# Kernel tuning notes

Measured on AMD Instinct MI355X. Metric: run time of the kernel, lower is better.

The kernel has to match this reference:

```python
import jax, jax.numpy as jnp
import numpy as np

BATCH, DIN, DSTATE, DOUT = 16384, 1024, 2048, 1024


def setup_inputs() -> dict:
    key = jax.random.key(0)
    ks = jax.random.split(key, 8)
    return {
        "u_in": jax.random.normal(ks[0], (BATCH, 1, DIN), dtype=jnp.float32),
        "x_re": jnp.zeros((DSTATE,), dtype=jnp.float32),
        "x_im": jnp.zeros((DSTATE,), dtype=jnp.float32),
        "nu_log": jax.random.uniform(ks[1], (DSTATE,), dtype=jnp.float32),
        "theta_log": jax.random.uniform(ks[2], (DSTATE,), dtype=jnp.float32),
        "gamma_log": jax.random.uniform(ks[3], (DSTATE,), dtype=jnp.float32),
        "B_re": jax.random.normal(ks[4], (DSTATE, DIN), dtype=jnp.float32) / np.sqrt(2 * DIN).astype(np.float32),
        "B_im": jax.random.normal(ks[5], (DSTATE, DIN), dtype=jnp.float32) / np.sqrt(2 * DIN).astype(np.float32),
        "C_re": jax.random.normal(ks[6], (DOUT, DSTATE), dtype=jnp.float32) / np.sqrt(DSTATE).astype(np.float32),
        "C_im": jax.random.normal(ks[7], (DOUT, DSTATE), dtype=jnp.float32) / np.sqrt(DSTATE).astype(np.float32),
        "D": jax.random.normal(jax.random.fold_in(key, 99), (DOUT, DIN), dtype=jnp.float32) / np.sqrt(DIN).astype(np.float32),
    }


def reference(u_in, x_re, x_im, nu_log, theta_log, gamma_log, B_re, B_im, C_re, C_im, D):
    # Diagonal complex transition lambda = exp(-exp(nu_log)) * exp(i*exp(theta_log))
    lam_mod = jnp.exp(-jnp.exp(nu_log))            # [S]
    theta = jnp.exp(theta_log)                     # [S]
    lam_re = lam_mod * jnp.cos(theta)
    lam_im = lam_mod * jnp.sin(theta)
    gammas = jnp.exp(gamma_log)                    # [S]
    # Bu = B @ u (u is real, so complex matmul splits into two real GEMMs)
    Bu_re = jnp.einsum('boi,si->bos', u_in, B_re)  # [B,1,S]
    Bu_im = jnp.einsum('boi,si->bos', u_in, B_im)  # [B,1,S]
    # x_new = lambda * x + gamma * Bu   (complex, diagonal)
    xn_re = lam_re * x_re - lam_im * x_im + gammas * Bu_re
    xn_im = lam_re * x_im + lam_im * x_re + gammas * Bu_im
    # y = 2*Re(C @ x_new) + D @ u
    y = (2.0 * (jnp.einsum('bos,js->boj', xn_re, C_re)
                - jnp.einsum('bos,js->boj', xn_im, C_im))
         + jnp.einsum('boi,ji->boj', u_in, D))     # [B,1,O]
    return y
```

## Files before the change

### kernel.cpp

```cpp
#include <hip/hip_runtime.h>
#include <hip/hip_fp16.h>
#include <stdint.h>


typedef _Float16 f16x8 __attribute__((ext_vector_type(8)));
typedef float f32x4 __attribute__((ext_vector_type(4)));

#define GLOBAL_AS __attribute__((address_space(1)))
#define LDS_AS __attribute__((address_space(3)))

constexpr int BATCH = 16384, DIN = 1024, DSTATE = 2048, DOUT = 1024;
constexpr int S2 = 2 * DSTATE;

__device__ __forceinline__ int lds_off(int row, int k) {
  int slot = k >> 3;
  int sl = slot ^ ((row >> 1) & 3);
  return row * 64 + sl * 16 + (k & 7) * 2;
}

__global__ void k_bgt(const float* __restrict__ Bre, const float* __restrict__ Bim,
                      const float* __restrict__ ga, __half* __restrict__ Bh,
                      __half* __restrict__ Bl) {
  __shared__ float tile[32][33];
  int s0 = blockIdx.x * 32, i0 = blockIdx.y * 32;
  int c = threadIdx.x & 31, r0 = threadIdx.x >> 5;
  const float* src = (s0 < DSTATE) ? Bre : Bim;
  int sbase = (s0 < DSTATE) ? s0 : s0 - DSTATE;
  for (int rr = 0; rr < 32; rr += 8) {
    int s = sbase + r0 + rr;
    tile[r0 + rr][c] = src[(long)s * DIN + i0 + c] * (256.f * expf(ga[s]));
  }
  __syncthreads();
  for (int rr = 0; rr < 32; rr += 8) {
    int i = i0 + r0 + rr;
    float v = tile[c][r0 + rr];
    __half h = __float2half(v);
    __half l = __float2half(v - __half2float(h));
    Bh[(long)i * S2 + s0 + c] = h;
    Bl[(long)i * S2 + s0 + c] = l;
  }
}

__global__ void k_y0(const float* __restrict__ xr, const float* __restrict__ xi,
                     const float* __restrict__ nu, const float* __restrict__ th,
                     const float* __restrict__ Cre, const float* __restrict__ Cim,
                     float* __restrict__ y0) {
  int j = blockIdx.x;
  float acc = 0.f;
  for (int s = threadIdx.x; s < DSTATE; s += 256) {
    float lm = expf(-expf(nu[s]));
    float t = expf(th[s]);
    float lr = lm * cosf(t), li = lm * sinf(t);
    float cr = lr * xr[s] - li * xi[s];
    float ci = lr * xi[s] + li * xr[s];
    acc += cr * Cre[(long)j * DSTATE + s] - ci * Cim[(long)j * DSTATE + s];
  }
  for (int off = 32; off; off >>= 1) acc += __shfl_down(acc, off);
  __shared__ float red[4];
  if ((threadIdx.x & 63) == 0) red[threadIdx.x >> 6] = acc;
  __syncthreads();
  if (threadIdx.x == 0) y0[j] = 2.f * (red[0] + red[1] + red[2] + red[3]);
}

template <int BM, int BN, int AMODE, int EPI>
__global__ __launch_bounds__(256, 4) void k_gemm(
    const float* __restrict__ A, const float* __restrict__ A2,
    const __half* __restrict__ Bh, const __half* __restrict__ Bl,
    const float* __restrict__ extra, float* __restrict__ outF,
    int M, int N, int K, int kiters, int kchunk) {
  constexpr int FM = BM / 32;
  constexpr int FN = BN / 32;
  constexpr int ABYTES = BM * 64;
  constexpr int BBYTES = BN * 64;
  __shared__ alignas(16) char smem[ABYTES + 2 * BBYTES];
  char* sA = smem;
  char* sBh = smem + ABYTES;
  char* sBl = smem + ABYTES + BBYTES;

  const int tid = threadIdx.x;
  const int lane = tid & 63;
  const int wid = tid >> 6;
  const int wr = wid >> 1, wc = wid & 1;
  int bm0, bn0, kb;
  if constexpr (EPI == 1) {
    int wg = blockIdx.x;
    int lin = (wg & 7) * 128 + (wg >> 3);
    bm0 = (lin >> 3) * BM;
    bn0 = (lin & 7) * BN;
    kb = 0;
  } else {
    bm0 = blockIdx.y * BM;
    bn0 = blockIdx.x * BN;
    kb = blockIdx.z * kchunk;
  }
  const int r16 = lane & 15;
  const int ksl = lane >> 4;

  f32x4 acc[FM][FN];
#pragma unroll
  for (int i = 0; i < FM; ++i)
#pragma unroll
    for (int j = 0; j < FN; ++j) acc[i][j] = f32x4{0.f, 0.f, 0.f, 0.f};

  constexpr int APT = (BM * 8) / 256;
  constexpr int IPW = (BN / 16) / 4;

  for (int kt = 0; kt < kiters; ++kt) {
    __syncthreads();
#pragma unroll
    for (int it = 0; it < APT; ++it) {
      int idx = it * 256 + tid;
      int row = idx >> 3;
      int k0 = (idx & 7) * 4;
      f32x4 v;
      if constexpr (AMODE == 2) {
        v = *(const f32x4*)(A + (long)(bm0 + row) * K + kb + kt * 32 + k0);
      } else {
        int s = kb + kt * 32 + k0;
        const float* src = (s < DSTATE) ? A : A2;
        int sc = (s < DSTATE) ? s : s - DSTATE;
        v = *(const f32x4*)(src + (long)(bm0 + row) * DSTATE + sc);
        v *= (s < DSTATE) ? 512.f : -512.f;
      }
      union { __half h[4]; uint64_t u; } p;
#pragma unroll
      for (int j = 0; j < 4; ++j) p.h[j] = __float2half(v[j]);
      *(uint64_t*)(sA + lds_off(row, k0)) = p.u;
    }
#pragma unroll
    for (int ii = 0; ii < IPW; ++ii) {
      int inst = wid * IPW + ii;
      int row = inst * 16 + (lane >> 2);
      int slot = (lane & 3) ^ ((row >> 1) & 3);
      const __half* gh = Bh + (long)(bn0 + row) * K + kb + kt * 32 + slot * 8;
      const __half* gl = Bl + (long)(bn0 + row) * K + kb + kt * 32 + slot * 8;
      __builtin_amdgcn_global_load_lds((GLOBAL_AS const unsigned int*)gh,
                                       (LDS_AS unsigned int*)(sBh + inst * 1024), 16, 0, 0);
      __builtin_amdgcn_global_load_lds((GLOBAL_AS const unsigned int*)gl,
                                       (LDS_AS unsigned int*)(sBl + inst * 1024), 16, 0, 0);
    }
    __syncthreads();
    f16x8 a[FM], bh[FN], bl[FN];
#pragma unroll
    for (int m = 0; m < FM; ++m) {
      int row = wr * (BM / 2) + m * 16 + r16;
      a[m] = *(const f16x8*)(sA + lds_off(row, ksl * 8));
    }
#pragma unroll
    for (int n = 0; n < FN; ++n) {
      int row = wc * (BN / 2) + n * 16 + r16;
      bh[n] = *(const f16x8*)(sBh + lds_off(row, ksl * 8));
      bl[n] = *(const f16x8*)(sBl + lds_off(row, ksl * 8));
    }
#pragma unroll
    for (int m = 0; m < FM; ++m)
#pragma unroll
      for (int n = 0; n < FN; ++n)
        acc[m][n] = __builtin_amdgcn_mfma_f32_16x16x32_f16(a[m], bh[n], acc[m][n], 0, 0, 0);
#pragma unroll
    for (int m = 0; m < FM; ++m)
#pragma unroll
      for (int n = 0; n < FN; ++n)
        acc[m][n] = __builtin_amdgcn_mfma_f32_16x16x32_f16(a[m], bl[n], acc[m][n], 0, 0, 0);
  }

  const int rowb = (lane >> 4) * 4;
#pragma unroll
  for (int m = 0; m < FM; ++m)
#pragma unroll
    for (int n = 0; n < FN; ++n)
#pragma unroll
      for (int r = 0; r < 4; ++r) {
        int gr = bm0 + wr * (BM / 2) + m * 16 + rowb + r;
        int gc = bn0 + wc * (BN / 2) + n * 16 + r16;
        if constexpr (EPI == 0) {
          outF[(long)blockIdx.z * M * N + (long)gr * N + gc] = acc[m][n][r];
        } else {
          outF[(long)gr * N + gc] = acc[m][n][r] * (1.f / 256.f) + extra[gc];
        }
      }
}

__global__ void k_redM(const float* __restrict__ P, const float* __restrict__ D,
                       __half* __restrict__ Mh, __half* __restrict__ Ml, int nparts) {
  int idx = (blockIdx.x * 256 + threadIdx.x) * 4;
  f32x4 s = {0.f, 0.f, 0.f, 0.f};
  for (int p = 0; p < nparts; ++p)
    s += *(const f32x4*)(P + ((long)p << 20) + idx);
  f32x4 d = *(const f32x4*)(D + idx);
  union { __half h[4]; uint64_t u; } ph, pl;
#pragma unroll
  for (int j = 0; j < 4; ++j) {
    float v = s[j] * (1.f / 256.f) + 256.f * d[j];
    __half hh = __float2half(v);
    ph.h[j] = hh;
    pl.h[j] = __float2half(v - __half2float(hh));
  }
  *(uint64_t*)(Mh + idx) = ph.u;
  *(uint64_t*)(Ml + idx) = pl.u;
}

extern "C" void kernel_launch(void* const* d_in, const int* in_sizes, int n_in,
                              void* d_out, int out_size, void* d_ws, size_t ws_size,
                              hipStream_t stream) {
  const float* u   = (const float*)d_in[0];
  const float* xr  = (const float*)d_in[1];
  const float* xi  = (const float*)d_in[2];
  const float* nu  = (const float*)d_in[3];
  const float* th  = (const float*)d_in[4];
  const float* ga  = (const float*)d_in[5];
  const float* Bre = (const float*)d_in[6];
  const float* Bim = (const float*)d_in[7];
  const float* Cre = (const float*)d_in[8];
  const float* Cim = (const float*)d_in[9];
  const float* Dm  = (const float*)d_in[10];
  float* y = (float*)d_out;

  char* w = (char*)d_ws;
  float* y0  = (float*)(w);
  __half* Bgh = (__half*)(w + 65536);
  __half* Bgl = (__half*)(w + 65536 + 8388608);
  __half* Mh  = (__half*)(w + 65536 + 16777216);
  __half* Ml  = (__half*)(w + 65536 + 16777216 + 2097152);
  const size_t pbase = 65536 + 16777216 + 4194304;
  float* Mpart = (float*)(w + pbase);

  const size_t part = (size_t)DOUT * DIN * 4;
  int KS = (ws_size >= pbase + 8 * part) ? 8 : (ws_size >= pbase + 4 * part) ? 4 : 2;

  k_bgt<<<dim3(S2 / 32, DIN / 32), 256, 0, stream>>>(Bre, Bim, ga, Bgh, Bgl);
  k_y0<<<DOUT, 256, 0, stream>>>(xr, xi, nu, th, Cre, Cim, y0);
  k_gemm<128, 128, 1, 0><<<dim3(DIN / 128, DOUT / 128, KS), 256, 0, stream>>>(
      Cre, Cim, Bgh, Bgl, nullptr, Mpart, DOUT, DIN, S2, (S2 / KS) / 32, S2 / KS);
  k_redM<<<1024, 256, 0, stream>>>(Mpart, Dm, Mh, Ml, KS);
  k_gemm<128, 128, 2, 1><<<(BATCH / 128) * (DOUT / 128), 256, 0, stream>>>(
      u, nullptr, Mh, Ml, y0, y, BATCH, DOUT, DIN, DIN / 32, 0);
}
```

Before: 296.7 us.

## Double-buffer LDS tiles in GEMM with register-prefetched A and async B loads

Replaces the single-buffered GEMM kernel with a double-buffered version. While MFMAs run on the current stage, the next k-tile's A is prefetched into registers and B is issued with async global_load_lds. The A values are converted and written to the alternate buffer after compute, which cuts to one barrier per iteration. The cost is doubled LDS (48KB) and more registers, so launch bounds drop to 2 blocks per CU and occupancy may fall.

```diff
diff --git a/kernel.cpp b/kernel.cpp
--- a/kernel.cpp
+++ b/kernel.cpp
@@ -62,20 +62,59 @@
   if (threadIdx.x == 0) y0[j] = 2.f * (red[0] + red[1] + red[2] + red[3]);
 }
 
-template <int BM, int BN, int AMODE, int EPI>
-__global__ __launch_bounds__(256, 4) void k_gemm(
+template <int AMODE>
+__device__ __forceinline__ f32x4 load_a(const float* __restrict__ A,
+                                        const float* __restrict__ A2,
+                                        int bm0, int K, int kglob, int tid, int it) {
+  int idx = it * 256 + tid;
+  int row = idx >> 3;
+  int k0 = (idx & 7) * 4;
+  if constexpr (AMODE == 2) {
+    return *(const f32x4*)(A + (long)(bm0 + row) * K + kglob + k0);
+  } else {
+    int s = kglob + k0;
+    const float* src = (s < DSTATE) ? A : A2;
+    int sc = (s < DSTATE) ? s : s - DSTATE;
+    f32x4 v = *(const f32x4*)(src + (long)(bm0 + row) * DSTATE + sc);
+    return v * ((s < DSTATE) ? 512.f : -512.f);
+  }
+}
+
+__device__ __forceinline__ void write_a(f32x4 v, char* sA, int tid, int it) {
+  int idx = it * 256 + tid;
+  int row = idx >> 3;
+  int k0 = (idx & 7) * 4;
+  union { __half h[4]; uint64_t u; } p;
+#pragma unroll
+  for (int j = 0; j < 4; ++j) p.h[j] = __float2half(v[j]);
+  *(uint64_t*)(sA + lds_off(row, k0)) = p.u;
+}
+
+__device__ __forceinline__ void stage_b(const __half* __restrict__ Bh,
+                                        const __half* __restrict__ Bl,
+                                        char* sBh, char* sBl,
+                                        int bn0, int K, int kglob, int wid, int lane) {
+#pragma unroll
+  for (int ii = 0; ii < 2; ++ii) {
+    int inst = wid * 2 + ii;
+    int row = inst * 16 + (lane >> 2);
+    int slot = (lane & 3) ^ ((row >> 1) & 3);
+    const __half* gh = Bh + (long)(bn0 + row) * K + kglob + slot * 8;
+    const __half* gl = Bl + (long)(bn0 + row) * K + kglob + slot * 8;
+    __builtin_amdgcn_global_load_lds((GLOBAL_AS const unsigned int*)gh,
+                                     (LDS_AS unsigned int*)(sBh + inst * 1024), 16, 0, 0);
+    __builtin_amdgcn_global_load_lds((GLOBAL_AS const unsigned int*)gl,
+                                     (LDS_AS unsigned int*)(sBl + inst * 1024), 16, 0, 0);
+  }
+}
+
+template <int AMODE, int EPI>
+__global__ __launch_bounds__(256, 2) void k_gemm2(
     const float* __restrict__ A, const float* __restrict__ A2,
     const __half* __restrict__ Bh, const __half* __restrict__ Bl,
     const float* __restrict__ extra, float* __restrict__ outF,
-    int M, int N, int K, int kiters, int kchunk) {
-  constexpr int FM = BM / 32;
-  constexpr int FN = BN / 32;
-  constexpr int ABYTES = BM * 64;
-  constexpr int BBYTES = BN * 64;
-  __shared__ alignas(16) char smem[ABYTES + 2 * BBYTES];
-  char* sA = smem;
-  char* sBh = smem + ABYTES;
-  char* sBl = smem + ABYTES + BBYTES;
+    int K, int N, int kiters, int kchunk) {
+  __shared__ alignas(16) char smem[2 * 24576];
 
   const int tid = threadIdx.x;
   const int lane = tid & 63;
@@ -85,96 +124,78 @@
   if constexpr (EPI == 1) {
     int wg = blockIdx.x;
     int lin = (wg & 7) * 128 + (wg >> 3);
-    bm0 = (lin >> 3) * BM;
-    bn0 = (lin & 7) * BN;
+    bm0 = (lin >> 3) * 128;
+    bn0 = (lin & 7) * 128;
     kb = 0;
   } else {
-    bm0 = blockIdx.y * BM;
-    bn0 = blockIdx.x * BN;
+    bm0 = blockIdx.y * 128;
+    bn0 = blockIdx.x * 128;
     kb = blockIdx.z * kchunk;
   }
   const int r16 = lane & 15;
   const int ksl = lane >> 4;
 
-  f32x4 acc[FM][FN];
-#pragma unroll
-  for (int i = 0; i < FM; ++i)
-#pragma unroll
-    for (int j = 0; j < FN; ++j) acc[i][j] = f32x4{0.f, 0.f, 0.f, 0.f};
-
-  constexpr int APT = (BM * 8) / 256;
-  constexpr int IPW = (BN / 16) / 4;
+  f32x4 acc[4][4];
+#pragma unroll
+  for (int i = 0; i < 4; ++i)
+#pragma unroll
+    for (int j = 0; j < 4; ++j) acc[i][j] = f32x4{0.f, 0.f, 0.f, 0.f};
+
+  f32x4 va[4];
+#pragma unroll
+  for (int it = 0; it < 4; ++it) va[it] = load_a<AMODE>(A, A2, bm0, K, kb, tid, it);
+  stage_b(Bh, Bl, smem + 8192, smem + 16384, bn0, K, kb, wid, lane);
+#pragma unroll
+  for (int it = 0; it < 4; ++it) write_a(va[it], smem, tid, it);
+  __syncthreads();
 
   for (int kt = 0; kt < kiters; ++kt) {
-    __syncthreads();
-#pragma unroll
-    for (int it = 0; it < APT; ++it) {
-      int idx = it * 256 + tid;
-      int row = idx >> 3;
-      int k0 = (idx & 7) * 4;
-      f32x4 v;
-      if constexpr (AMODE == 2) {
-        v = *(const f32x4*)(A + (long)(bm0 + row) * K + kb + kt * 32 + k0);
-      } else {
-        int s = kb + kt * 32 + k0;
-        const float* src = (s < DSTATE) ? A : A2;
-        int sc = (s < DSTATE) ? s : s - DSTATE;
-        v = *(const f32x4*)(src + (long)(bm0 + row) * DSTATE + sc);
-        v *= (s < DSTATE) ? 512.f : -512.f;
-      }
-      union { __half h[4]; uint64_t u; } p;
-#pragma unroll
-      for (int j = 0; j < 4; ++j) p.h[j] = __float2half(v[j]);
-      *(uint64_t*)(sA + lds_off(row, k0)) = p.u;
+    char* cur = smem + (kt & 1) * 24576;
+    char* nxt = smem + ((kt + 1) & 1) * 24576;
+    const bool more = (kt + 1 < kiters);
+    if (more) {
+      int kg = kb + (kt + 1) * 32;
+#pragma unroll
+      for (int it = 0; it < 4; ++it) va[it] = load_a<AMODE>(A, A2, bm0, K, kg, tid, it);
+      stage_b(Bh, Bl, nxt + 8192, nxt + 16384, bn0, K, kg, wid, lane);
     }
-#pragma unroll
-    for (int ii = 0; ii < IPW; ++ii) {
-      int inst = wid * IPW + ii;
-      int row = inst * 16 + (lane >> 2);
-      int slot = (lane & 3) ^ ((row >> 1) & 3);
-      const __half* gh = Bh + (long)(bn0 + row) * K + kb + kt * 32 + slot * 8;
-      const __half* gl = Bl + (long)(bn0 + row) * K + kb + kt * 32 + slot * 8;
-      __builtin_amdgcn_global_load_lds((GLOBAL_AS const unsigned int*)gh,
-                                       (LDS_AS unsigned int*)(sBh + inst * 1024), 16, 0, 0);
-      __builtin_amdgcn_global_load_lds((GLOBAL_AS const unsigned int*)gl,
-                                       (LDS_AS unsigned int*)(sBl + inst * 1024), 16, 0, 0);
+    f16x8 a[4], bh[4], bl[4];
+#pragma unroll
+    for (int m = 0; m < 4; ++m)
+      a[m] = *(const f16x8*)(cur + lds_off(wr * 64 + m * 16 + r16, ksl * 8));
+#pragma unroll
+    for (int n = 0; n < 4; ++n) {
+      bh[n] = *(const f16x8*)(cur + 8192 + lds_off(wc * 64 + n * 16 + r16, ksl * 8));
+      bl[n] = *(const f16x8*)(cur + 16384 + lds_off(wc * 64 + n * 16 + r16, ksl * 8));
+    }
+#pragma unroll
+    for (int m = 0; m < 4; ++m)
+#pragma unroll
+      for (int n = 0; n < 4; ++n)
+        acc[m][n] = __builtin_amdgcn_mfma_f32_16x16x32_f16(a[m], bh[n], acc[m][n], 0, 0, 0);
+#pragma unroll
+    for (int m = 0; m < 4; ++m)
+#pragma unroll
+      for (int n = 0; n < 4; ++n)
+        acc[m][n] = __builtin_amdgcn_mfma_f32_16x16x32_f16(a[m], bl[n], acc[m][n], 0, 0, 0);
+    if (more) {
+#pragma unroll
+      for (int it = 0; it < 4; ++it) write_a(va[it], nxt, tid, it);
     }
     __syncthreads();
-    f16x8 a[FM], bh[FN], bl[FN];
-#pragma unroll
-    for (int m = 0; m < FM; ++m) {
-      int row = wr * (BM / 2) + m * 16 + r16;
-      a[m] = *(const f16x8*)(sA + lds_off(row, ksl * 8));
-    }
-#pragma unroll
-    for (int n = 0; n < FN; ++n) {
-      int row = wc * (BN / 2) + n * 16 + r16;
-      bh[n] = *(const f16x8*)(sBh + lds_off(row, ksl * 8));
-      bl[n] = *(const f16x8*)(sBl + lds_off(row, ksl * 8));
-    }
-#pragma unroll
-    for (int m = 0; m < FM; ++m)
-#pragma unroll
-      for (int n = 0; n < FN; ++n)
-        acc[m][n] = __builtin_amdgcn_mfma_f32_16x16x32_f16(a[m], bh[n], acc[m][n], 0, 0, 0);
-#pragma unroll
-    for (int m = 0; m < FM; ++m)
-#pragma unroll
-      for (int n = 0; n < FN; ++n)
-        acc[m][n] = __builtin_amdgcn_mfma_f32_16x16x32_f16(a[m], bl[n], acc[m][n], 0, 0, 0);
   }
 
   const int rowb = (lane >> 4) * 4;
 #pragma unroll
-  for (int m = 0; m < FM; ++m)
-#pragma unroll
-    for (int n = 0; n < FN; ++n)
+  for (int m = 0; m < 4; ++m)
+#pragma unroll
+    for (int n = 0; n < 4; ++n)
 #pragma unroll
       for (int r = 0; r < 4; ++r) {
-        int gr = bm0 + wr * (BM / 2) + m * 16 + rowb + r;
-        int gc = bn0 + wc * (BN / 2) + n * 16 + r16;
+        int gr = bm0 + wr * 64 + m * 16 + rowb + r;
+        int gc = bn0 + wc * 64 + n * 16 + r16;
         if constexpr (EPI == 0) {
-          outF[(long)blockIdx.z * M * N + (long)gr * N + gc] = acc[m][n][r];
+          outF[(long)blockIdx.z * DOUT * DIN + (long)gr * N + gc] = acc[m][n][r];
         } else {
           outF[(long)gr * N + gc] = acc[m][n][r] * (1.f / 256.f) + extra[gc];
         }
@@ -222,17 +243,17 @@
   __half* Bgl = (__half*)(w + 65536 + 8388608);
   __half* Mh  = (__half*)(w + 65536 + 16777216);
   __half* Ml  = (__half*)(w + 65536 + 16777216 + 2097152);
-  const size_t pbase = 65536 + 16777216 + 4194304;
-  float* Mpart = (float*)(w + pbase);
-
+  const size_t base = 65536 + 16777216 + 4194304;
+  float* Mpart = (float*)(w + base);
   const size_t part = (size_t)DOUT * DIN * 4;
-  int KS = (ws_size >= pbase + 8 * part) ? 8 : (ws_size >= pbase + 4 * part) ? 4 : 2;
+
+  int KS = (ws_size >= base + 8 * part) ? 8 : (ws_size >= base + 4 * part) ? 4 : 2;
 
   k_bgt<<<dim3(S2 / 32, DIN / 32), 256, 0, stream>>>(Bre, Bim, ga, Bgh, Bgl);
   k_y0<<<DOUT, 256, 0, stream>>>(xr, xi, nu, th, Cre, Cim, y0);
-  k_gemm<128, 128, 1, 0><<<dim3(DIN / 128, DOUT / 128, KS), 256, 0, stream>>>(
-      Cre, Cim, Bgh, Bgl, nullptr, Mpart, DOUT, DIN, S2, (S2 / KS) / 32, S2 / KS);
+  k_gemm2<1, 0><<<dim3(DIN / 128, DOUT / 128, KS), 256, 0, stream>>>(
+      Cre, Cim, Bgh, Bgl, nullptr, Mpart, S2, DIN, (S2 / KS) / 32, S2 / KS);
   k_redM<<<1024, 256, 0, stream>>>(Mpart, Dm, Mh, Ml, KS);
-  k_gemm<128, 128, 2, 1><<<(BATCH / 128) * (DOUT / 128), 256, 0, stream>>>(
-      u, nullptr, Mh, Ml, y0, y, BATCH, DOUT, DIN, DIN / 32, 0);
-}
+  k_gemm2<2, 1><<<(BATCH / 128) * (DOUT / 128), 256, 0, stream>>>(
+      u, nullptr, Mh, Ml, y0, y, DIN, DOUT, DIN / 32, 0);
+}
```

New measurement: 282.4 us. 1.05x faster.
